# Optimization experiments

Measured on AMD Instinct MI355X. Metric: run time of the kernel, lower is better.

The kernel has to match this reference:

```python
import jax, jax.numpy as jnp
import numpy as np

N = 10000
E = 160000
UNITS = 64
NUM_RBF = 32
CUTOFF = 1.0


def _xavier(k, shape):
    fan_out, fan_in = shape
    lim = float(np.sqrt(6.0 / (fan_in + fan_out)))
    return jax.random.uniform(k, shape, minval=-lim, maxval=lim, dtype=jnp.float32)


def setup_inputs() -> dict:
    key = jax.random.key(0)
    ks = jax.random.split(key, 16)
    inp = {
        "edge_index": jax.random.randint(ks[0], (2, E), 0, N),
        "edge_weight": jax.random.uniform(ks[1], (E,), dtype=jnp.float32),
        "edge_attr": jax.random.normal(ks[2], (E, NUM_RBF), dtype=jnp.float32),
        "X": jax.random.normal(ks[3], (N, UNITS, 3, 3), dtype=jnp.float32),
        # scalar MLP: num_rbf -> units -> 2*units -> 3*units
        "Ws0": _xavier(ks[4], (UNITS, NUM_RBF)), "bs0": jnp.zeros((UNITS,), jnp.float32),
        "Ws1": _xavier(ks[5], (2 * UNITS, UNITS)), "bs1": jnp.zeros((2 * UNITS,), jnp.float32),
        "Ws2": _xavier(ks[6], (3 * UNITS, 2 * UNITS)), "bs2": jnp.zeros((3 * UNITS,), jnp.float32),
    }
    for i in range(6):
        inp[f"Wt{i}"] = _xavier(ks[7 + i], (UNITS, UNITS))
    return inp


def cosine_cutoff(r, cutoff):
    return jnp.where(r < cutoff, 0.5 * (jnp.cos(jnp.pi * r / cutoff) + 1.0), 0.0)


def tensor_norm(X):
    # X: [N, units, 3, 3] -> [N, units]
    return jnp.sum(X * X, axis=(-2, -1))


def decompose_tensor(X):
    eye = jnp.eye(3, dtype=X.dtype)
    trace = jnp.trace(X, axis1=-2, axis2=-1)  # [N, units]
    I = (trace / 3.0)[..., None, None] * eye
    A = 0.5 * (X - jnp.swapaxes(X, -2, -1))
    S = 0.5 * (X + jnp.swapaxes(X, -2, -1)) - I
    return I, A, S


def channel_linear(T, W):
    # linear over the channel dim: [N, c, 3, 3] x [d, c] -> [N, d, 3, 3]
    return jnp.einsum('ncij,dc->ndij', T, W)


def reference(edge_index, edge_weight, edge_attr, X,
              Ws0, bs0, Ws1, bs1, Ws2, bs2,
              Wt0, Wt1, Wt2, Wt3, Wt4, Wt5):
    act = jax.nn.silu
    C = cosine_cutoff(edge_weight, CUTOFF)  # [E]
    h = act(edge_attr @ Ws0.T + bs0)
    h = act(h @ Ws1.T + bs1)
    h = act(h @ Ws2.T + bs2)  # [E, 3*units]
    ea = (h * C[:, None]).reshape(h.shape[0], UNITS, 3)  # [E, units, 3]

    X = X / (tensor_norm(X) + 1.0)[..., None, None]
    I, A, S = decompose_tensor(X)
    I = channel_linear(I, Wt0)
    A = channel_linear(A, Wt1)
    S = channel_linear(S, Wt2)
    Y = I + A + S

    src, dst = edge_index[0], edge_index[1]
    n = X.shape[0]
    # message = per-edge radial scaling of gathered node tensors; aggregate at src
    Im = jax.ops.segment_sum(ea[..., 0, None, None] * I[dst], src, num_segments=n)
    Am = jax.ops.segment_sum(ea[..., 1, None, None] * A[dst], src, num_segments=n)
    Sm = jax.ops.segment_sum(ea[..., 2, None, None] * S[dst], src, num_segments=n)
    msg = Im + Am + Sm

    # O(3): symmetrized product of batched 3x3 matmuls
    AB = jnp.matmul(msg, Y) + jnp.matmul(Y, msg)
    I2, A2, S2 = decompose_tensor(AB)
    normp1 = (tensor_norm(I2 + A2 + S2) + 1.0)[..., None, None]
    I2 = channel_linear(I2 / normp1, Wt3)
    A2 = channel_linear(A2 / normp1, Wt4)
    S2 = channel_linear(S2 / normp1, Wt5)
    dX = I2 + A2 + S2
    return X + dX + jnp.matmul(dX, dX)
```

## Files before the change

### kernel.cpp

```cpp
#include <hip/hip_runtime.h>
#include <math.h>

#define NN 10000
#define EE 160000

#define OFF_WTT 0
#define OFF_PK  24576
#define OFF_B2P 41984
#define OFF_IASH 42176
#define OFF_EAH 3242176
#define OFF_ATTRP 18602176
#define OFF_CP  21162176
#define OFF_INT 21322176

typedef __attribute__((ext_vector_type(8))) _Float16 h16x8;
typedef __attribute__((ext_vector_type(2))) __fp16 fp16x2_raw;
typedef __attribute__((ext_vector_type(4))) float f32x4;

__device__ __forceinline__ float silu_f(float x) {
    return x * __builtin_amdgcn_rcpf(1.0f + __expf(-x));
}
__device__ __forceinline__ unsigned int pkh(float a, float b) {
    union { fp16x2_raw h; unsigned int u; } cv;
    cv.h = __builtin_amdgcn_cvt_pkrtz(a, b);
    return cv.u;
}
__device__ __forceinline__ unsigned short f2h(float f) {
    union { _Float16 h; unsigned short u; } cv; cv.h = (_Float16)f; return cv.u;
}
__device__ __forceinline__ float h2f(unsigned short s) {
    union { unsigned short u; _Float16 h; } cv; cv.u = s; return (float)cv.h;
}
__device__ __forceinline__ float h2f_lo(unsigned int u) { return h2f((unsigned short)(u & 0xffffu)); }
__device__ __forceinline__ float h2f_hi(unsigned int u) { return h2f((unsigned short)(u >> 16)); }
__device__ __forceinline__ unsigned int bperm(int addr, unsigned int v) {
    return (unsigned int)__builtin_amdgcn_ds_bpermute(addr, (int)v);
}

__global__ void k_prep(const float* __restrict__ Wt0, const float* __restrict__ Wt1,
                       const float* __restrict__ Wt2, const float* __restrict__ Wt3,
                       const float* __restrict__ Wt4, const float* __restrict__ Wt5,
                       const float* __restrict__ Ws0, const float* __restrict__ Ws1,
                       const float* __restrict__ Ws2, const float* __restrict__ bs2,
                       const int* __restrict__ ei,
                       float* __restrict__ WtT, unsigned short* __restrict__ PK,
                       float* __restrict__ bs2p, int* __restrict__ counts) {
    int idx = blockIdx.x * 256 + threadIdx.x;
    if (idx < 24576) {
        int k = idx >> 12, r = idx & 4095;
        int c = r >> 6, d = r & 63;
        const float* W = (k == 0) ? Wt0 : (k == 1) ? Wt1 : (k == 2) ? Wt2
                       : (k == 3) ? Wt3 : (k == 4) ? Wt4 : Wt5;
        WtT[idx] = W[d * 64 + c];
    } else if (idx < 26624) {
        int q = idx - 24576;
        int ot = q >> 9, r = q & 511, lane = r >> 3, j = r & 7;
        int k = ((lane >> 4) * 8) + j, o = ot * 16 + (lane & 15);
        PK[q] = f2h(Ws0[o * 32 + k]);
    } else if (idx < 34816) {
        int q = idx - 24576;
        int i = q - 2048, ch = i >> 9, r = i & 511, lane = r >> 3, j = r & 7;
        int ot = ch >> 1, ks = ch & 1;
        int k = ks * 32 + (lane >> 4) * 8 + j, o = ot * 16 + (lane & 15);
        PK[q] = f2h(Ws1[o * 64 + k]);
    } else if (idx < 59392) {
        int q = idx - 24576;
        int i = q - 10240, ch = i >> 9, r = i & 511, lane = r >> 3, j = r & 7;
        int ot = ch >> 2, ks = ch & 3;
        int k = ks * 32 + (lane >> 4) * 8 + j;
        int op = ot * 16 + (lane & 15);
        int o = (op & 63) * 3 + (op >> 6);
        PK[q] = f2h(Ws2[o * 128 + k]);
    } else if (idx < 59584) {
        int op = idx - 59392;
        bs2p[op] = bs2[(op & 63) * 3 + (op >> 6)];
    } else if (idx < 59584 + EE) {
        int e = idx - 59584;
        atomicAdd(&counts[ei[e]], 1);
    }
}

__global__ __launch_bounds__(256) void k_scan(const int* __restrict__ counts,
                                              int* __restrict__ offsets) {
    __shared__ int sums[256];
    int t = threadIdx.x;
    int base = t * 40;
    int s = 0;
    if (base < NN) {
        const int4* p = (const int4*)(counts + base);
#pragma unroll
        for (int q = 0; q < 10; ++q) { int4 a = p[q]; s += a.x + a.y + a.z + a.w; }
    }
    sums[t] = s;
    __syncthreads();
    for (int off = 1; off < 256; off <<= 1) {
        int tmp = (t >= off) ? sums[t - off] : 0;
        __syncthreads();
        sums[t] += tmp;
        __syncthreads();
    }
    int run = sums[t] - s;
    if (base < NN) {
        const int4* p = (const int4*)(counts + base);
#pragma unroll
        for (int q = 0; q < 10; ++q) {
            int4 a = p[q];
            offsets[base + 4 * q + 0] = run; run += a.x;
            offsets[base + 4 * q + 1] = run; run += a.y;
            offsets[base + 4 * q + 2] = run; run += a.z;
            offsets[base + 4 * q + 3] = run; run += a.w;
        }
    }
    if (t == 255) offsets[NN] = run;
}

__global__ void k_fill(const int* __restrict__ ei, const int* __restrict__ offsets,
                       const float* __restrict__ attr, const float* __restrict__ ew,
                       int* __restrict__ cursor, int* __restrict__ dstp,
                       unsigned short* __restrict__ attrP, float* __restrict__ Cp) {
    int e = blockIdx.x * 256 + threadIdx.x;
    if (e < EE) {
        int s = ei[e];
        int pos = offsets[s] + atomicAdd(&cursor[s], 1);
        dstp[pos] = ei[EE + e];
        const float4* ap = (const float4*)(attr + (size_t)e * 32);
        unsigned int pk[16];
#pragma unroll
        for (int q = 0; q < 8; ++q) {
            float4 v = ap[q];
            pk[2 * q]     = pkh(v.x, v.y);
            pk[2 * q + 1] = pkh(v.z, v.w);
        }
        uint4* dst = (uint4*)(attrP + (size_t)pos * 32);
#pragma unroll
        for (int q = 0; q < 4; ++q)
            dst[q] = make_uint4(pk[4 * q], pk[4 * q + 1], pk[4 * q + 2], pk[4 * q + 3]);
        float rw = ew[e];
        Cp[pos] = (rw < 1.0f) ? 0.5f * (cosf(3.14159265358979f * rw) + 1.0f) : 0.0f;
    }
}

__global__ __launch_bounds__(256) void k_nodeprep(const float* __restrict__ X,
                                                  const float* __restrict__ WtT,
                                                  unsigned int* __restrict__ IASu) {
    int t = threadIdx.x, w = t >> 6, c = t & 63;
    int n = blockIdx.x * 4 + w;
    __shared__ float XS[4][576];
    __shared__ float L[4][64][12];
    float* xs = XS[w];
#pragma unroll
    for (int i = 0; i < 9; i++) xs[c + 64 * i] = X[(size_t)n * 576 + c + 64 * i];
    __builtin_amdgcn_wave_barrier();
    float x[9];
#pragma unroll
    for (int j = 0; j < 9; j++) x[j] = xs[c * 9 + j];
    float nrm = 0.f;
#pragma unroll
    for (int j = 0; j < 9; j++) nrm += x[j] * x[j];
    float inv = __builtin_amdgcn_rcpf(nrm + 1.0f);
#pragma unroll
    for (int j = 0; j < 9; j++) x[j] *= inv;
    float tr3 = (x[0] + x[4] + x[8]) * (1.0f / 3.0f);
    L[w][c][0] = tr3;
    L[w][c][1] = 0.5f * (x[1] - x[3]);
    L[w][c][2] = 0.5f * (x[2] - x[6]);
    L[w][c][3] = 0.5f * (x[5] - x[7]);
    L[w][c][4] = x[0] - tr3;
    L[w][c][5] = x[4] - tr3;
    L[w][c][6] = 0.5f * (x[1] + x[3]);
    L[w][c][7] = 0.5f * (x[2] + x[6]);
    L[w][c][8] = 0.5f * (x[5] + x[7]);
    __builtin_amdgcn_wave_barrier();
    int d = c;
    const float* W0 = WtT;
    const float* W1 = WtT + 4096;
    const float* W2 = WtT + 8192;
    float aI = 0, aA0 = 0, aA1 = 0, aA2 = 0, aS0 = 0, aS1 = 0, aS2 = 0, aS3 = 0, aS4 = 0;
    for (int cc = 0; cc < 64; ++cc) {
        float w0 = W0[cc * 64 + d], w1 = W1[cc * 64 + d], w2 = W2[cc * 64 + d];
        float4 L0 = *(const float4*)&L[w][cc][0];
        float4 L1 = *(const float4*)&L[w][cc][4];
        float L8 = L[w][cc][8];
        aI  += w0 * L0.x;
        aA0 += w1 * L0.y; aA1 += w1 * L0.z; aA2 += w1 * L0.w;
        aS0 += w2 * L1.x; aS1 += w2 * L1.y; aS2 += w2 * L1.z;
        aS3 += w2 * L1.w; aS4 += w2 * L8;
    }
    unsigned int* op = IASu + (size_t)n * 320 + d;
    op[0]   = pkh(aI, aA0);
    op[64]  = pkh(aA1, aA2);
    op[128] = pkh(aS0, aS1);
    op[192] = pkh(aS2, aS3);
    op[256] = pkh(aS4, 0.0f);
}

__global__ __launch_bounds__(256) void k_mlp(const unsigned short* __restrict__ attrP,
                                             const float* __restrict__ Cp,
                                             const unsigned short* __restrict__ PK,
                                             const float* __restrict__ bs0,
                                             const float* __restrict__ bs1,
                                             const float* __restrict__ bs2p,
                                             unsigned short* __restrict__ eah) {
    int t = threadIdx.x, w = t >> 6, l = t & 63;
    int e = l & 15, lg = l >> 4;
    int pos = blockIdx.x * 64 + w * 16 + e;
    const h16x8* P1 = (const h16x8*)PK;
    const h16x8* P2 = (const h16x8*)(PK + 2048);
    const h16x8* P3 = (const h16x8*)(PK + 10240);
    union U8 { h16x8 h; unsigned int u[4]; uint4 v; };
    U8 B1;
    B1.v = *((const uint4*)(attrP + (size_t)pos * 32) + lg);
    float C = Cp[pos];
    int src0 = ((lg & 1) * 32 + e) * 4;
    int src1 = src0 + 64;
    bool hi = (lg >= 2);

    unsigned int h01[8], h23[8];
#pragma unroll
    for (int ot = 0; ot < 4; ++ot) {
        float4 bb = *(const float4*)&bs0[ot * 16 + lg * 4];
        f32x4 acc = {bb.x, bb.y, bb.z, bb.w};
        acc = __builtin_amdgcn_mfma_f32_16x16x32_f16(P1[ot * 64 + l], B1.h, acc, 0, 0, 0);
        h01[ot] = pkh(silu_f(acc[0]), silu_f(acc[1]));
        h23[ot] = pkh(silu_f(acc[2]), silu_f(acc[3]));
    }
    U8 B2a, B2b;
    {
        unsigned int a, b;
        a = bperm(src0, h01[0]); b = bperm(src0, h01[1]); B2a.u[0] = hi ? b : a;
        a = bperm(src0, h23[0]); b = bperm(src0, h23[1]); B2a.u[1] = hi ? b : a;
        a = bperm(src1, h01[0]); b = bperm(src1, h01[1]); B2a.u[2] = hi ? b : a;
        a = bperm(src1, h23[0]); b = bperm(src1, h23[1]); B2a.u[3] = hi ? b : a;
        a = bperm(src0, h01[2]); b = bperm(src0, h01[3]); B2b.u[0] = hi ? b : a;
        a = bperm(src0, h23[2]); b = bperm(src0, h23[3]); B2b.u[1] = hi ? b : a;
        a = bperm(src1, h01[2]); b = bperm(src1, h01[3]); B2b.u[2] = hi ? b : a;
        a = bperm(src1, h23[2]); b = bperm(src1, h23[3]); B2b.u[3] = hi ? b : a;
    }
#pragma unroll
    for (int ot = 0; ot < 8; ++ot) {
        float4 bb = *(const float4*)&bs1[ot * 16 + lg * 4];
        f32x4 acc = {bb.x, bb.y, bb.z, bb.w};
        acc = __builtin_amdgcn_mfma_f32_16x16x32_f16(P2[(ot * 2 + 0) * 64 + l], B2a.h, acc, 0, 0, 0);
        acc = __builtin_amdgcn_mfma_f32_16x16x32_f16(P2[(ot * 2 + 1) * 64 + l], B2b.h, acc, 0, 0, 0);
        h01[ot] = pkh(silu_f(acc[0]), silu_f(acc[1]));
        h23[ot] = pkh(silu_f(acc[2]), silu_f(acc[3]));
    }
    U8 B3[4];
#pragma unroll
    for (int ks = 0; ks < 4; ++ks) {
        unsigned int a, b;
        a = bperm(src0, h01[ks * 2]); b = bperm(src0, h01[ks * 2 + 1]); B3[ks].u[0] = hi ? b : a;
        a = bperm(src0, h23[ks * 2]); b = bperm(src0, h23[ks * 2 + 1]); B3[ks].u[1] = hi ? b : a;
        a = bperm(src1, h01[ks * 2]); b = bperm(src1, h01[ks * 2 + 1]); B3[ks].u[2] = hi ? b : a;
        a = bperm(src1, h23[ks * 2]); b = bperm(src1, h23[ks * 2 + 1]); B3[ks].u[3] = hi ? b : a;
    }
    size_t ebase = (size_t)pos * 192;
#pragma unroll
    for (int ot = 0; ot < 12; ++ot) {
        float4 bb = *(const float4*)&bs2p[ot * 16 + lg * 4];
        f32x4 acc = {bb.x, bb.y, bb.z, bb.w};
        acc = __builtin_amdgcn_mfma_f32_16x16x32_f16(P3[(ot * 4 + 0) * 64 + l], B3[0].h, acc, 0, 0, 0);
        acc = __builtin_amdgcn_mfma_f32_16x16x32_f16(P3[(ot * 4 + 1) * 64 + l], B3[1].h, acc, 0, 0, 0);
        acc = __builtin_amdgcn_mfma_f32_16x16x32_f16(P3[(ot * 4 + 2) * 64 + l], B3[2].h, acc, 0, 0, 0);
        acc = __builtin_amdgcn_mfma_f32_16x16x32_f16(P3[(ot * 4 + 3) * 64 + l], B3[3].h, acc, 0, 0, 0);
        unsigned int u01 = pkh(silu_f(acc[0]) * C, silu_f(acc[1]) * C);
        unsigned int u23 = pkh(silu_f(acc[2]) * C, silu_f(acc[3]) * C);
        *(uint2*)&eah[ebase + ot * 16 + lg * 4] = make_uint2(u01, u23);
    }
}

__global__ __launch_bounds__(256) void k_aggout(const int* __restrict__ offsets,
                                                const int* __restrict__ dstp,
                                                const unsigned short* __restrict__ eah,
                                                const unsigned int* __restrict__ IASu,
                                                const float* __restrict__ X,
                                                const float* __restrict__ WtT,
                                                float* __restrict__ out) {
    int t = threadIdx.x, w = t >> 6, c = t & 63;
    int n = blockIdx.x * 4 + w;
    __shared__ float XS[4][576];
    __shared__ float LO[4][768];
    float* xs = XS[w];
    float* lo = LO[w];
#pragma unroll
    for (int i = 0; i < 9; i++) xs[c + 64 * i] = X[(size_t)n * 576 + c + 64 * i];

    int beg = offsets[n], end = offsets[n + 1];
    float m0 = 0, m1 = 0, m2 = 0, m3 = 0, m4 = 0, m5 = 0, m6 = 0, m7 = 0, m8 = 0;
    int i = beg;
    for (; i + 4 <= end; i += 4) {
        float a[4][3];
        unsigned int u[4][5];
#pragma unroll
        for (int q = 0; q < 4; ++q) {
            const unsigned short* ep = eah + (size_t)(i + q) * 192;
            a[q][0] = h2f(ep[c]); a[q][1] = h2f(ep[64 + c]); a[q][2] = h2f(ep[128 + c]);
            const unsigned int* p = IASu + (size_t)dstp[i + q] * 320 + c;
            u[q][0] = p[0]; u[q][1] = p[64]; u[q][2] = p[128]; u[q][3] = p[192]; u[q][4] = p[256];
        }
#pragma unroll
        for (int q = 0; q < 4; ++q) {
            m0 += a[q][0] * h2f_lo(u[q][0]); m1 += a[q][1] * h2f_hi(u[q][0]);
            m2 += a[q][1] * h2f_lo(u[q][1]); m3 += a[q][1] * h2f_hi(u[q][1]);
            m4 += a[q][2] * h2f_lo(u[q][2]); m5 += a[q][2] * h2f_hi(u[q][2]);
            m6 += a[q][2] * h2f_lo(u[q][3]); m7 += a[q][2] * h2f_hi(u[q][3]);
            m8 += a[q][2] * h2f_lo(u[q][4]);
        }
    }
    for (; i < end; ++i) {
        const unsigned short* ep = eah + (size_t)i * 192;
        float a0 = h2f(ep[c]), a1 = h2f(ep[64 + c]), a2 = h2f(ep[128 + c]);
        const unsigned int* p = IASu + (size_t)dstp[i] * 320 + c;
        unsigned int u0 = p[0], u1 = p[64], u2 = p[128], u3 = p[192], u4 = p[256];
        m0 += a0 * h2f_lo(u0); m1 += a1 * h2f_hi(u0);
        m2 += a1 * h2f_lo(u1); m3 += a1 * h2f_hi(u1);
        m4 += a2 * h2f_lo(u2); m5 += a2 * h2f_hi(u2);
        m6 += a2 * h2f_lo(u3); m7 += a2 * h2f_hi(u3);
        m8 += a2 * h2f_lo(u4);
    }
    const unsigned int* yp = IASu + (size_t)n * 320 + c;
    unsigned int y0 = yp[0], y1 = yp[64], y2 = yp[128], y3 = yp[192], y4 = yp[256];
    float yI = h2f_lo(y0), yA0 = h2f_hi(y0), yA1 = h2f_lo(y1), yA2 = h2f_hi(y1);
    float yS0 = h2f_lo(y2), yS1 = h2f_hi(y2), yS2 = h2f_lo(y3), yS3 = h2f_hi(y3);
    float yS4 = h2f_lo(y4);

    float M[3][3] = {
        { m0 + m4,   m1 + m6,  m2 + m7 },
        { -m1 + m6,  m0 + m5,  m3 + m8 },
        { -m2 + m7, -m3 + m8,  m0 - m4 - m5 } };
    float Y[3][3] = {
        { yI + yS0,   yA0 + yS2,  yA1 + yS3 },
        { -yA0 + yS2, yI + yS1,   yA2 + yS4 },
        { -yA1 + yS3, -yA2 + yS4, yI - yS0 - yS1 } };
    float AB[3][3];
#pragma unroll
    for (int ii = 0; ii < 3; ii++)
#pragma unroll
        for (int j = 0; j < 3; j++) {
            float s = 0.f;
#pragma unroll
            for (int k = 0; k < 3; k++) s += M[ii][k] * Y[k][j] + Y[ii][k] * M[k][j];
            AB[ii][j] = s;
        }
    float tr3 = (AB[0][0] + AB[1][1] + AB[2][2]) * (1.0f / 3.0f);
    float fro = 0.f;
#pragma unroll
    for (int ii = 0; ii < 3; ii++)
#pragma unroll
        for (int j = 0; j < 3; j++) fro += AB[ii][j] * AB[ii][j];
    float inv = __builtin_amdgcn_rcpf(fro + 1.0f);
    float (*L12)[12] = (float (*)[12])lo;
    L12[c][0] = tr3 * inv;
    L12[c][1] = 0.5f * (AB[0][1] - AB[1][0]) * inv;
    L12[c][2] = 0.5f * (AB[0][2] - AB[2][0]) * inv;
    L12[c][3] = 0.5f * (AB[1][2] - AB[2][1]) * inv;
    L12[c][4] = (AB[0][0] - tr3) * inv;
    L12[c][5] = (AB[1][1] - tr3) * inv;
    L12[c][6] = 0.5f * (AB[0][1] + AB[1][0]) * inv;
    L12[c][7] = 0.5f * (AB[0][2] + AB[2][0]) * inv;
    L12[c][8] = 0.5f * (AB[1][2] + AB[2][1]) * inv;
    __builtin_amdgcn_wave_barrier();
    int d = c;
    const float* W3 = WtT + 3 * 4096;
    const float* W4 = WtT + 4 * 4096;
    const float* W5 = WtT + 5 * 4096;
    float aI = 0, aA0 = 0, aA1 = 0, aA2 = 0, aS0 = 0, aS1 = 0, aS2 = 0, aS3 = 0, aS4 = 0;
    for (int cc = 0; cc < 64; ++cc) {
        float w3 = W3[cc * 64 + d], w4 = W4[cc * 64 + d], w5 = W5[cc * 64 + d];
        float4 L0 = *(const float4*)&L12[cc][0];
        float4 L1 = *(const float4*)&L12[cc][4];
        float L8 = L12[cc][8];
        aI  += w3 * L0.x;
        aA0 += w4 * L0.y; aA1 += w4 * L0.z; aA2 += w4 * L0.w;
        aS0 += w5 * L1.x; aS1 += w5 * L1.y; aS2 += w5 * L1.z;
        aS3 += w5 * L1.w; aS4 += w5 * L8;
    }
    float dX[3][3] = {
        { aI + aS0,   aA0 + aS2,  aA1 + aS3 },
        { -aA0 + aS2, aI + aS1,   aA2 + aS4 },
        { -aA1 + aS3, -aA2 + aS4, aI - aS0 - aS1 } };
    float D2[3][3];
#pragma unroll
    for (int ii = 0; ii < 3; ii++)
#pragma unroll
        for (int j = 0; j < 3; j++) {
            float s = 0.f;
#pragma unroll
            for (int k = 0; k < 3; k++) s += dX[ii][k] * dX[k][j];
            D2[ii][j] = s;
        }
    float x[9];
    __builtin_amdgcn_wave_barrier();
#pragma unroll
    for (int j = 0; j < 9; j++) x[j] = xs[d * 9 + j];
    float nrm = 0.f;
#pragma unroll
    for (int j = 0; j < 9; j++) nrm += x[j] * x[j];
    float xinv = __builtin_amdgcn_rcpf(nrm + 1.0f);
    __builtin_amdgcn_wave_barrier();
#pragma unroll
    for (int ii = 0; ii < 3; ii++)
#pragma unroll
        for (int j = 0; j < 3; j++)
            lo[d * 9 + ii * 3 + j] = x[ii * 3 + j] * xinv + dX[ii][j] + D2[ii][j];
    __builtin_amdgcn_wave_barrier();
#pragma unroll
    for (int ii = 0; ii < 9; ii++) out[(size_t)n * 576 + c + 64 * ii] = lo[c + 64 * ii];
}

extern "C" void kernel_launch(void* const* d_in, const int* in_sizes, int n_in,
                              void* d_out, int out_size, void* d_ws, size_t ws_size,
                              hipStream_t stream) {
    (void)in_sizes; (void)n_in; (void)out_size; (void)ws_size;
    const int* ei = (const int*)d_in[0];
    const float* ew = (const float*)d_in[1];
    const float* attr = (const float*)d_in[2];
    const float* X = (const float*)d_in[3];
    const float* Ws0 = (const float*)d_in[4];
    const float* bs0 = (const float*)d_in[5];
    const float* Ws1 = (const float*)d_in[6];
    const float* bs1 = (const float*)d_in[7];
    const float* Ws2 = (const float*)d_in[8];
    const float* bs2 = (const float*)d_in[9];
    const float* Wt0 = (const float*)d_in[10];
    const float* Wt1 = (const float*)d_in[11];
    const float* Wt2 = (const float*)d_in[12];
    const float* Wt3 = (const float*)d_in[13];
    const float* Wt4 = (const float*)d_in[14];
    const float* Wt5 = (const float*)d_in[15];
    float* ws = (float*)d_ws;
    int* ibase = (int*)(ws + OFF_INT);
    int* counts = ibase;
    int* cursor = ibase + NN;
    int* offsets = ibase + 2 * NN;
    int* dstp = ibase + 3 * NN + 1;
    unsigned short* PK = (unsigned short*)(ws + OFF_PK);
    unsigned int* IASu = (unsigned int*)(ws + OFF_IASH);
    unsigned short* eah = (unsigned short*)(ws + OFF_EAH);
    unsigned short* attrP = (unsigned short*)(ws + OFF_ATTRP);
    float* Cp = ws + OFF_CP;

    (void)hipMemsetAsync(counts, 0, 2 * NN * sizeof(int), stream);
    k_prep<<<(59584 + EE + 255) / 256, 256, 0, stream>>>(
        Wt0, Wt1, Wt2, Wt3, Wt4, Wt5, Ws0, Ws1, Ws2, bs2, ei,
        ws, PK, ws + OFF_B2P, counts);
    k_scan<<<1, 256, 0, stream>>>(counts, offsets);
    k_fill<<<(EE + 255) / 256, 256, 0, stream>>>(ei, offsets, attr, ew, cursor, dstp, attrP, Cp);
    k_nodeprep<<<NN / 4, 256, 0, stream>>>(X, ws, IASu);
    k_mlp<<<EE / 64, 256, 0, stream>>>(attrP, Cp, PK, bs0, bs1, ws + OFF_B2P, eah);
    k_aggout<<<NN / 4, 256, 0, stream>>>(offsets, dstp, eah, IASu, X, ws, (float*)d_out);
}
```

Measured before the change: 160.0 us.

## Run edge MLP in original edge order and gather via bucket index in aggregation

The fill kernel no longer permutes and converts edge attributes and cutoff values into sorted order. It only records the original edge id per sorted slot. The MLP now reads fp32 attributes and edge weights directly in original order, converting to fp16 and computing the cosine cutoff itself. The aggregation kernel gathers per-edge MLP outputs through the bucket indirection instead of reading them contiguously, and gains an 8-way unrolled loop for more loads in flight. This removes a scatter and an intermediate buffer but makes the eah reads in aggregation random.

```diff
diff --git a/kernel.cpp b/kernel.cpp
--- a/kernel.cpp
+++ b/kernel.cpp
@@ -9,9 +9,7 @@
 #define OFF_B2P 41984
 #define OFF_IASH 42176
 #define OFF_EAH 3242176
-#define OFF_ATTRP 18602176
-#define OFF_CP  21162176
-#define OFF_INT 21322176
+#define OFF_INT 18602176
 
 typedef __attribute__((ext_vector_type(8))) _Float16 h16x8;
 typedef __attribute__((ext_vector_type(2))) __fp16 fp16x2_raw;
@@ -115,28 +113,14 @@
 }
 
 __global__ void k_fill(const int* __restrict__ ei, const int* __restrict__ offsets,
-                       const float* __restrict__ attr, const float* __restrict__ ew,
-                       int* __restrict__ cursor, int* __restrict__ dstp,
-                       unsigned short* __restrict__ attrP, float* __restrict__ Cp) {
+                       int* __restrict__ cursor, int* __restrict__ bucket,
+                       int* __restrict__ dstp) {
     int e = blockIdx.x * 256 + threadIdx.x;
     if (e < EE) {
         int s = ei[e];
         int pos = offsets[s] + atomicAdd(&cursor[s], 1);
+        bucket[pos] = e;
         dstp[pos] = ei[EE + e];
-        const float4* ap = (const float4*)(attr + (size_t)e * 32);
-        unsigned int pk[16];
-#pragma unroll
-        for (int q = 0; q < 8; ++q) {
-            float4 v = ap[q];
-            pk[2 * q]     = pkh(v.x, v.y);
-            pk[2 * q + 1] = pkh(v.z, v.w);
-        }
-        uint4* dst = (uint4*)(attrP + (size_t)pos * 32);
-#pragma unroll
-        for (int q = 0; q < 4; ++q)
-            dst[q] = make_uint4(pk[4 * q], pk[4 * q + 1], pk[4 * q + 2], pk[4 * q + 3]);
-        float rw = ew[e];
-        Cp[pos] = (rw < 1.0f) ? 0.5f * (cosf(3.14159265358979f * rw) + 1.0f) : 0.0f;
     }
 }
 
@@ -194,8 +178,8 @@
     op[256] = pkh(aS4, 0.0f);
 }
 
-__global__ __launch_bounds__(256) void k_mlp(const unsigned short* __restrict__ attrP,
-                                             const float* __restrict__ Cp,
+__global__ __launch_bounds__(256) void k_mlp(const float* __restrict__ attr,
+                                             const float* __restrict__ ew,
                                              const unsigned short* __restrict__ PK,
                                              const float* __restrict__ bs0,
                                              const float* __restrict__ bs1,
@@ -209,8 +193,15 @@
     const h16x8* P3 = (const h16x8*)(PK + 10240);
     union U8 { h16x8 h; unsigned int u[4]; uint4 v; };
     U8 B1;
-    B1.v = *((const uint4*)(attrP + (size_t)pos * 32) + lg);
-    float C = Cp[pos];
+    {
+        const float* ap = attr + (size_t)pos * 32 + lg * 8;
+        float4 a0 = *(const float4*)ap;
+        float4 a1 = *(const float4*)(ap + 4);
+        B1.u[0] = pkh(a0.x, a0.y); B1.u[1] = pkh(a0.z, a0.w);
+        B1.u[2] = pkh(a1.x, a1.y); B1.u[3] = pkh(a1.z, a1.w);
+    }
+    float rw = ew[pos];
+    float C = (rw < 1.0f) ? 0.5f * (cosf(3.14159265358979f * rw) + 1.0f) : 0.0f;
     int src0 = ((lg & 1) * 32 + e) * 4;
     int src1 = src0 + 64;
     bool hi = (lg >= 2);
@@ -270,6 +261,7 @@
 }
 
 __global__ __launch_bounds__(256) void k_aggout(const int* __restrict__ offsets,
+                                                const int* __restrict__ bucket,
                                                 const int* __restrict__ dstp,
                                                 const unsigned short* __restrict__ eah,
                                                 const unsigned int* __restrict__ IASu,
@@ -288,12 +280,31 @@
     int beg = offsets[n], end = offsets[n + 1];
     float m0 = 0, m1 = 0, m2 = 0, m3 = 0, m4 = 0, m5 = 0, m6 = 0, m7 = 0, m8 = 0;
     int i = beg;
+    for (; i + 8 <= end; i += 8) {
+        float a[8][3];
+        unsigned int u[8][5];
+#pragma unroll
+        for (int q = 0; q < 8; ++q) {
+            const unsigned short* ep = eah + (size_t)bucket[i + q] * 192;
+            a[q][0] = h2f(ep[c]); a[q][1] = h2f(ep[64 + c]); a[q][2] = h2f(ep[128 + c]);
+            const unsigned int* p = IASu + (size_t)dstp[i + q] * 320 + c;
+            u[q][0] = p[0]; u[q][1] = p[64]; u[q][2] = p[128]; u[q][3] = p[192]; u[q][4] = p[256];
+        }
+#pragma unroll
+        for (int q = 0; q < 8; ++q) {
+            m0 += a[q][0] * h2f_lo(u[q][0]); m1 += a[q][1] * h2f_hi(u[q][0]);
+            m2 += a[q][1] * h2f_lo(u[q][1]); m3 += a[q][1] * h2f_hi(u[q][1]);
+            m4 += a[q][2] * h2f_lo(u[q][2]); m5 += a[q][2] * h2f_hi(u[q][2]);
+            m6 += a[q][2] * h2f_lo(u[q][3]); m7 += a[q][2] * h2f_hi(u[q][3]);
+            m8 += a[q][2] * h2f_lo(u[q][4]);
+        }
+    }
     for (; i + 4 <= end; i += 4) {
         float a[4][3];
         unsigned int u[4][5];
 #pragma unroll
         for (int q = 0; q < 4; ++q) {
-            const unsigned short* ep = eah + (size_t)(i + q) * 192;
+            const unsigned short* ep = eah + (size_t)bucket[i + q] * 192;
             a[q][0] = h2f(ep[c]); a[q][1] = h2f(ep[64 + c]); a[q][2] = h2f(ep[128 + c]);
             const unsigned int* p = IASu + (size_t)dstp[i + q] * 320 + c;
             u[q][0] = p[0]; u[q][1] = p[64]; u[q][2] = p[128]; u[q][3] = p[192]; u[q][4] = p[256];
@@ -308,7 +319,7 @@
         }
     }
     for (; i < end; ++i) {
-        const unsigned short* ep = eah + (size_t)i * 192;
+        const unsigned short* ep = eah + (size_t)bucket[i] * 192;
         float a0 = h2f(ep[c]), a1 = h2f(ep[64 + c]), a2 = h2f(ep[128 + c]);
         const unsigned int* p = IASu + (size_t)dstp[i] * 320 + c;
         unsigned int u0 = p[0], u1 = p[64], u2 = p[128], u3 = p[192], u4 = p[256];
@@ -433,20 +444,19 @@
     int* counts = ibase;
     int* cursor = ibase + NN;
     int* offsets = ibase + 2 * NN;
-    int* dstp = ibase + 3 * NN + 1;
+    int* bucket = ibase + 3 * NN + 1;
+    int* dstp = bucket + EE;
     unsigned short* PK = (unsigned short*)(ws + OFF_PK);
     unsigned int* IASu = (unsigned int*)(ws + OFF_IASH);
     unsigned short* eah = (unsigned short*)(ws + OFF_EAH);
-    unsigned short* attrP = (unsigned short*)(ws + OFF_ATTRP);
-    float* Cp = ws + OFF_CP;
 
     (void)hipMemsetAsync(counts, 0, 2 * NN * sizeof(int), stream);
     k_prep<<<(59584 + EE + 255) / 256, 256, 0, stream>>>(
         Wt0, Wt1, Wt2, Wt3, Wt4, Wt5, Ws0, Ws1, Ws2, bs2, ei,
         ws, PK, ws + OFF_B2P, counts);
     k_scan<<<1, 256, 0, stream>>>(counts, offsets);
-    k_fill<<<(EE + 255) / 256, 256, 0, stream>>>(ei, offsets, attr, ew, cursor, dstp, attrP, Cp);
+    k_fill<<<(EE + 255) / 256, 256, 0, stream>>>(ei, offsets, cursor, bucket, dstp);
     k_nodeprep<<<NN / 4, 256, 0, stream>>>(X, ws, IASu);
-    k_mlp<<<EE / 64, 256, 0, stream>>>(attrP, Cp, PK, bs0, bs1, ws + OFF_B2P, eah);
-    k_aggout<<<NN / 4, 256, 0, stream>>>(offsets, dstp, eah, IASu, X, ws, (float*)d_out);
-}
+    k_mlp<<<EE / 64, 256, 0, stream>>>(attr, ew, PK, bs0, bs1, ws + OFF_B2P, eah);
+    k_aggout<<<NN / 4, 256, 0, stream>>>(offsets, bucket, dstp, eah, IASu, X, ws, (float*)d_out);
+}
```

Result: no change. 161.9 us (+1.2%).

## Merge node-prep and edge MLP into one launch; shuffle-broadcast dst indices

Applied to the files above, without the earlier changes.

Folds the node-preparation kernel and the edge MLP kernel into a single launch whose block index picks which job each block does, so one launch and its tail disappear and the two independent workloads can overlap on the GPU. In the aggregation kernel each wave now loads up to 64 destination indices at once and broadcasts them with shuffles, replacing repeated scalar-dependent global loads inside the gather loop. The fused kernel reserves the larger node-prep shared memory for every block, which may reduce occupancy for the MLP blocks.

```diff
diff --git a/kernel.cpp b/kernel.cpp
--- a/kernel.cpp
+++ b/kernel.cpp
@@ -140,132 +140,133 @@
     }
 }
 
-__global__ __launch_bounds__(256) void k_nodeprep(const float* __restrict__ X,
-                                                  const float* __restrict__ WtT,
-                                                  unsigned int* __restrict__ IASu) {
-    int t = threadIdx.x, w = t >> 6, c = t & 63;
-    int n = blockIdx.x * 4 + w;
-    __shared__ float XS[4][576];
-    __shared__ float L[4][64][12];
-    float* xs = XS[w];
-#pragma unroll
-    for (int i = 0; i < 9; i++) xs[c + 64 * i] = X[(size_t)n * 576 + c + 64 * i];
-    __builtin_amdgcn_wave_barrier();
-    float x[9];
-#pragma unroll
-    for (int j = 0; j < 9; j++) x[j] = xs[c * 9 + j];
-    float nrm = 0.f;
-#pragma unroll
-    for (int j = 0; j < 9; j++) nrm += x[j] * x[j];
-    float inv = __builtin_amdgcn_rcpf(nrm + 1.0f);
-#pragma unroll
-    for (int j = 0; j < 9; j++) x[j] *= inv;
-    float tr3 = (x[0] + x[4] + x[8]) * (1.0f / 3.0f);
-    L[w][c][0] = tr3;
-    L[w][c][1] = 0.5f * (x[1] - x[3]);
-    L[w][c][2] = 0.5f * (x[2] - x[6]);
-    L[w][c][3] = 0.5f * (x[5] - x[7]);
-    L[w][c][4] = x[0] - tr3;
-    L[w][c][5] = x[4] - tr3;
-    L[w][c][6] = 0.5f * (x[1] + x[3]);
-    L[w][c][7] = 0.5f * (x[2] + x[6]);
-    L[w][c][8] = 0.5f * (x[5] + x[7]);
-    __builtin_amdgcn_wave_barrier();
-    int d = c;
-    const float* W0 = WtT;
-    const float* W1 = WtT + 4096;
-    const float* W2 = WtT + 8192;
-    float aI = 0, aA0 = 0, aA1 = 0, aA2 = 0, aS0 = 0, aS1 = 0, aS2 = 0, aS3 = 0, aS4 = 0;
-    for (int cc = 0; cc < 64; ++cc) {
-        float w0 = W0[cc * 64 + d], w1 = W1[cc * 64 + d], w2 = W2[cc * 64 + d];
-        float4 L0 = *(const float4*)&L[w][cc][0];
-        float4 L1 = *(const float4*)&L[w][cc][4];
-        float L8 = L[w][cc][8];
-        aI  += w0 * L0.x;
-        aA0 += w1 * L0.y; aA1 += w1 * L0.z; aA2 += w1 * L0.w;
-        aS0 += w2 * L1.x; aS1 += w2 * L1.y; aS2 += w2 * L1.z;
-        aS3 += w2 * L1.w; aS4 += w2 * L8;
-    }
-    unsigned int* op = IASu + (size_t)n * 320 + d;
-    op[0]   = pkh(aI, aA0);
-    op[64]  = pkh(aA1, aA2);
-    op[128] = pkh(aS0, aS1);
-    op[192] = pkh(aS2, aS3);
-    op[256] = pkh(aS4, 0.0f);
-}
-
-__global__ __launch_bounds__(256) void k_mlp(const unsigned short* __restrict__ attrP,
-                                             const float* __restrict__ Cp,
-                                             const unsigned short* __restrict__ PK,
-                                             const float* __restrict__ bs0,
-                                             const float* __restrict__ bs1,
-                                             const float* __restrict__ bs2p,
-                                             unsigned short* __restrict__ eah) {
+__global__ __launch_bounds__(256) void k_mlpnp(const unsigned short* __restrict__ attrP,
+                                               const float* __restrict__ Cp,
+                                               const unsigned short* __restrict__ PK,
+                                               const float* __restrict__ bs0,
+                                               const float* __restrict__ bs1,
+                                               const float* __restrict__ bs2p,
+                                               const float* __restrict__ X,
+                                               const float* __restrict__ WtT,
+                                               unsigned short* __restrict__ eah,
+                                               unsigned int* __restrict__ IASu) {
+    __shared__ float SH[4][1344];
     int t = threadIdx.x, w = t >> 6, l = t & 63;
-    int e = l & 15, lg = l >> 4;
-    int pos = blockIdx.x * 64 + w * 16 + e;
-    const h16x8* P1 = (const h16x8*)PK;
-    const h16x8* P2 = (const h16x8*)(PK + 2048);
-    const h16x8* P3 = (const h16x8*)(PK + 10240);
-    union U8 { h16x8 h; unsigned int u[4]; uint4 v; };
-    U8 B1;
-    B1.v = *((const uint4*)(attrP + (size_t)pos * 32) + lg);
-    float C = Cp[pos];
-    int src0 = ((lg & 1) * 32 + e) * 4;
-    int src1 = src0 + 64;
-    bool hi = (lg >= 2);
-
-    unsigned int h01[8], h23[8];
-#pragma unroll
-    for (int ot = 0; ot < 4; ++ot) {
-        float4 bb = *(const float4*)&bs0[ot * 16 + lg * 4];
-        f32x4 acc = {bb.x, bb.y, bb.z, bb.w};
-        acc = __builtin_amdgcn_mfma_f32_16x16x32_f16(P1[ot * 64 + l], B1.h, acc, 0, 0, 0);
-        h01[ot] = pkh(silu_f(acc[0]), silu_f(acc[1]));
-        h23[ot] = pkh(silu_f(acc[2]), silu_f(acc[3]));
-    }
-    U8 B2a, B2b;
-    {
-        unsigned int a, b;
-        a = bperm(src0, h01[0]); b = bperm(src0, h01[1]); B2a.u[0] = hi ? b : a;
-        a = bperm(src0, h23[0]); b = bperm(src0, h23[1]); B2a.u[1] = hi ? b : a;
-        a = bperm(src1, h01[0]); b = bperm(src1, h01[1]); B2a.u[2] = hi ? b : a;
-        a = bperm(src1, h23[0]); b = bperm(src1, h23[1]); B2a.u[3] = hi ? b : a;
-        a = bperm(src0, h01[2]); b = bperm(src0, h01[3]); B2b.u[0] = hi ? b : a;
-        a = bperm(src0, h23[2]); b = bperm(src0, h23[3]); B2b.u[1] = hi ? b : a;
-        a = bperm(src1, h01[2]); b = bperm(src1, h01[3]); B2b.u[2] = hi ? b : a;
-        a = bperm(src1, h23[2]); b = bperm(src1, h23[3]); B2b.u[3] = hi ? b : a;
-    }
-#pragma unroll
-    for (int ot = 0; ot < 8; ++ot) {
-        float4 bb = *(const float4*)&bs1[ot * 16 + lg * 4];
-        f32x4 acc = {bb.x, bb.y, bb.z, bb.w};
-        acc = __builtin_amdgcn_mfma_f32_16x16x32_f16(P2[(ot * 2 + 0) * 64 + l], B2a.h, acc, 0, 0, 0);
-        acc = __builtin_amdgcn_mfma_f32_16x16x32_f16(P2[(ot * 2 + 1) * 64 + l], B2b.h, acc, 0, 0, 0);
-        h01[ot] = pkh(silu_f(acc[0]), silu_f(acc[1]));
-        h23[ot] = pkh(silu_f(acc[2]), silu_f(acc[3]));
-    }
-    U8 B3[4];
-#pragma unroll
-    for (int ks = 0; ks < 4; ++ks) {
-        unsigned int a, b;
-        a = bperm(src0, h01[ks * 2]); b = bperm(src0, h01[ks * 2 + 1]); B3[ks].u[0] = hi ? b : a;
-        a = bperm(src0, h23[ks * 2]); b = bperm(src0, h23[ks * 2 + 1]); B3[ks].u[1] = hi ? b : a;
-        a = bperm(src1, h01[ks * 2]); b = bperm(src1, h01[ks * 2 + 1]); B3[ks].u[2] = hi ? b : a;
-        a = bperm(src1, h23[ks * 2]); b = bperm(src1, h23[ks * 2 + 1]); B3[ks].u[3] = hi ? b : a;
-    }
-    size_t ebase = (size_t)pos * 192;
-#pragma unroll
-    for (int ot = 0; ot < 12; ++ot) {
-        float4 bb = *(const float4*)&bs2p[ot * 16 + lg * 4];
-        f32x4 acc = {bb.x, bb.y, bb.z, bb.w};
-        acc = __builtin_amdgcn_mfma_f32_16x16x32_f16(P3[(ot * 4 + 0) * 64 + l], B3[0].h, acc, 0, 0, 0);
-        acc = __builtin_amdgcn_mfma_f32_16x16x32_f16(P3[(ot * 4 + 1) * 64 + l], B3[1].h, acc, 0, 0, 0);
-        acc = __builtin_amdgcn_mfma_f32_16x16x32_f16(P3[(ot * 4 + 2) * 64 + l], B3[2].h, acc, 0, 0, 0);
-        acc = __builtin_amdgcn_mfma_f32_16x16x32_f16(P3[(ot * 4 + 3) * 64 + l], B3[3].h, acc, 0, 0, 0);
-        unsigned int u01 = pkh(silu_f(acc[0]) * C, silu_f(acc[1]) * C);
-        unsigned int u23 = pkh(silu_f(acc[2]) * C, silu_f(acc[3]) * C);
-        *(uint2*)&eah[ebase + ot * 16 + lg * 4] = make_uint2(u01, u23);
+    if (blockIdx.x < EE / 64) {
+        int e = l & 15, lg = l >> 4;
+        int pos = blockIdx.x * 64 + w * 16 + e;
+        const h16x8* P1 = (const h16x8*)PK;
+        const h16x8* P2 = (const h16x8*)(PK + 2048);
+        const h16x8* P3 = (const h16x8*)(PK + 10240);
+        union U8 { h16x8 h; unsigned int u[4]; uint4 v; };
+        U8 B1;
+        B1.v = *((const uint4*)(attrP + (size_t)pos * 32) + lg);
+        float C = Cp[pos];
+        int src0 = ((lg & 1) * 32 + e) * 4;
+        int src1 = src0 + 64;
+        bool hi = (lg >= 2);
+
+        unsigned int h01[8], h23[8];
+#pragma unroll
+        for (int ot = 0; ot < 4; ++ot) {
+            float4 bb = *(const float4*)&bs0[ot * 16 + lg * 4];
+            f32x4 acc = {bb.x, bb.y, bb.z, bb.w};
+            acc = __builtin_amdgcn_mfma_f32_16x16x32_f16(P1[ot * 64 + l], B1.h, acc, 0, 0, 0);
+            h01[ot] = pkh(silu_f(acc[0]), silu_f(acc[1]));
+            h23[ot] = pkh(silu_f(acc[2]), silu_f(acc[3]));
+        }
+        U8 B2a, B2b;
+        {
+            unsigned int a, b;
+            a = bperm(src0, h01[0]); b = bperm(src0, h01[1]); B2a.u[0] = hi ? b : a;
+            a = bperm(src0, h23[0]); b = bperm(src0, h23[1]); B2a.u[1] = hi ? b : a;
+            a = bperm(src1, h01[0]); b = bperm(src1, h01[1]); B2a.u[2] = hi ? b : a;
+            a = bperm(src1, h23[0]); b = bperm(src1, h23[1]); B2a.u[3] = hi ? b : a;
+            a = bperm(src0, h01[2]); b = bperm(src0, h01[3]); B2b.u[0] = hi ? b : a;
+            a = bperm(src0, h23[2]); b = bperm(src0, h23[3]); B2b.u[1] = hi ? b : a;
+            a = bperm(src1, h01[2]); b = bperm(src1, h01[3]); B2b.u[2] = hi ? b : a;
+            a = bperm(src1, h23[2]); b = bperm(src1, h23[3]); B2b.u[3] = hi ? b : a;
+        }
+#pragma unroll
+        for (int ot = 0; ot < 8; ++ot) {
+            float4 bb = *(const float4*)&bs1[ot * 16 + lg * 4];
+            f32x4 acc = {bb.x, bb.y, bb.z, bb.w};
+            acc = __builtin_amdgcn_mfma_f32_16x16x32_f16(P2[(ot * 2 + 0) * 64 + l], B2a.h, acc, 0, 0, 0);
+            acc = __builtin_amdgcn_mfma_f32_16x16x32_f16(P2[(ot * 2 + 1) * 64 + l], B2b.h, acc, 0, 0, 0);
+            h01[ot] = pkh(silu_f(acc[0]), silu_f(acc[1]));
+            h23[ot] = pkh(silu_f(acc[2]), silu_f(acc[3]));
+        }
+        U8 B3[4];
+#pragma unroll
+        for (int ks = 0; ks < 4; ++ks) {
+            unsigned int a, b;
+            a = bperm(src0, h01[ks * 2]); b = bperm(src0, h01[ks * 2 + 1]); B3[ks].u[0] = hi ? b : a;
+            a = bperm(src0, h23[ks * 2]); b = bperm(src0, h23[ks * 2 + 1]); B3[ks].u[1] = hi ? b : a;
+            a = bperm(src1, h01[ks * 2]); b = bperm(src1, h01[ks * 2 + 1]); B3[ks].u[2] = hi ? b : a;
+            a = bperm(src1, h23[ks * 2]); b = bperm(src1, h23[ks * 2 + 1]); B3[ks].u[3] = hi ? b : a;
+        }
+        size_t ebase = (size_t)pos * 192;
+#pragma unroll
+        for (int ot = 0; ot < 12; ++ot) {
+            float4 bb = *(const float4*)&bs2p[ot * 16 + lg * 4];
+            f32x4 acc = {bb.x, bb.y, bb.z, bb.w};
+            acc = __builtin_amdgcn_mfma_f32_16x16x32_f16(P3[(ot * 4 + 0) * 64 + l], B3[0].h, acc, 0, 0, 0);
+            acc = __builtin_amdgcn_mfma_f32_16x16x32_f16(P3[(ot * 4 + 1) * 64 + l], B3[1].h, acc, 0, 0, 0);
+            acc = __builtin_amdgcn_mfma_f32_16x16x32_f16(P3[(ot * 4 + 2) * 64 + l], B3[2].h, acc, 0, 0, 0);
+            acc = __builtin_amdgcn_mfma_f32_16x16x32_f16(P3[(ot * 4 + 3) * 64 + l], B3[3].h, acc, 0, 0, 0);
+            unsigned int u01 = pkh(silu_f(acc[0]) * C, silu_f(acc[1]) * C);
+            unsigned int u23 = pkh(silu_f(acc[2]) * C, silu_f(acc[3]) * C);
+            *(uint2*)&eah[ebase + ot * 16 + lg * 4] = make_uint2(u01, u23);
+        }
+    } else {
+        int c = l;
+        int n = (blockIdx.x - EE / 64) * 4 + w;
+        float* xs = SH[w];
+        float (*L12)[12] = (float (*)[12])(xs + 576);
+#pragma unroll
+        for (int i = 0; i < 9; i++) xs[c + 64 * i] = X[(size_t)n * 576 + c + 64 * i];
+        __builtin_amdgcn_wave_barrier();
+        float x[9];
+#pragma unroll
+        for (int j = 0; j < 9; j++) x[j] = xs[c * 9 + j];
+        float nrm = 0.f;
+#pragma unroll
+        for (int j = 0; j < 9; j++) nrm += x[j] * x[j];
+        float inv = __builtin_amdgcn_rcpf(nrm + 1.0f);
+#pragma unroll
+        for (int j = 0; j < 9; j++) x[j] *= inv;
+        float tr3 = (x[0] + x[4] + x[8]) * (1.0f / 3.0f);
+        L12[c][0] = tr3;
+        L12[c][1] = 0.5f * (x[1] - x[3]);
+        L12[c][2] = 0.5f * (x[2] - x[6]);
+        L12[c][3] = 0.5f * (x[5] - x[7]);
+        L12[c][4] = x[0] - tr3;
+        L12[c][5] = x[4] - tr3;
+        L12[c][6] = 0.5f * (x[1] + x[3]);
+        L12[c][7] = 0.5f * (x[2] + x[6]);
+        L12[c][8] = 0.5f * (x[5] + x[7]);
+        __builtin_amdgcn_wave_barrier();
+        int d = c;
+        const float* W0 = WtT;
+        const float* W1 = WtT + 4096;
+        const float* W2 = WtT + 8192;
+        float aI = 0, aA0 = 0, aA1 = 0, aA2 = 0, aS0 = 0, aS1 = 0, aS2 = 0, aS3 = 0, aS4 = 0;
+        for (int cc = 0; cc < 64; ++cc) {
+            float w0 = W0[cc * 64 + d], w1 = W1[cc * 64 + d], w2 = W2[cc * 64 + d];
+            float4 L0 = *(const float4*)&L12[cc][0];
+            float4 L1 = *(const float4*)&L12[cc][4];
+            float L8 = L12[cc][8];
+            aI  += w0 * L0.x;
+            aA0 += w1 * L0.y; aA1 += w1 * L0.z; aA2 += w1 * L0.w;
+            aS0 += w2 * L1.x; aS1 += w2 * L1.y; aS2 += w2 * L1.z;
+            aS3 += w2 * L1.w; aS4 += w2 * L8;
+        }
+        unsigned int* op = IASu + (size_t)n * 320 + d;
+        op[0]   = pkh(aI, aA0);
+        op[64]  = pkh(aA1, aA2);
+        op[128] = pkh(aS0, aS1);
+        op[192] = pkh(aS2, aS3);
+        op[256] = pkh(aS4, 0.0f);
     }
 }
 
@@ -286,16 +287,24 @@
     for (int i = 0; i < 9; i++) xs[c + 64 * i] = X[(size_t)n * 576 + c + 64 * i];
 
     int beg = offsets[n], end = offsets[n + 1];
+    int dv = 0;
+    { int idx = beg + c; if (idx < end) dv = dstp[idx]; }
     float m0 = 0, m1 = 0, m2 = 0, m3 = 0, m4 = 0, m5 = 0, m6 = 0, m7 = 0, m8 = 0;
     int i = beg;
     for (; i + 4 <= end; i += 4) {
+        int q0 = i - beg;
+        int d0 = (q0 < 64)     ? __shfl(dv, q0)     : dstp[i];
+        int d1 = (q0 + 1 < 64) ? __shfl(dv, q0 + 1) : dstp[i + 1];
+        int d2 = (q0 + 2 < 64) ? __shfl(dv, q0 + 2) : dstp[i + 2];
+        int d3 = (q0 + 3 < 64) ? __shfl(dv, q0 + 3) : dstp[i + 3];
+        int dd[4] = {d0, d1, d2, d3};
         float a[4][3];
         unsigned int u[4][5];
 #pragma unroll
         for (int q = 0; q < 4; ++q) {
             const unsigned short* ep = eah + (size_t)(i + q) * 192;
             a[q][0] = h2f(ep[c]); a[q][1] = h2f(ep[64 + c]); a[q][2] = h2f(ep[128 + c]);
-            const unsigned int* p = IASu + (size_t)dstp[i + q] * 320 + c;
+            const unsigned int* p = IASu + (size_t)dd[q] * 320 + c;
             u[q][0] = p[0]; u[q][1] = p[64]; u[q][2] = p[128]; u[q][3] = p[192]; u[q][4] = p[256];
         }
 #pragma unroll
@@ -308,9 +317,11 @@
         }
     }
     for (; i < end; ++i) {
+        int q0 = i - beg;
+        int dst = (q0 < 64) ? __shfl(dv, q0) : dstp[i];
         const unsigned short* ep = eah + (size_t)i * 192;
         float a0 = h2f(ep[c]), a1 = h2f(ep[64 + c]), a2 = h2f(ep[128 + c]);
-        const unsigned int* p = IASu + (size_t)dstp[i] * 320 + c;
+        const unsigned int* p = IASu + (size_t)dst * 320 + c;
         unsigned int u0 = p[0], u1 = p[64], u2 = p[128], u3 = p[192], u4 = p[256];
         m0 += a0 * h2f_lo(u0); m1 += a1 * h2f_hi(u0);
         m2 += a1 * h2f_lo(u1); m3 += a1 * h2f_hi(u1);
@@ -446,7 +457,7 @@
         ws, PK, ws + OFF_B2P, counts);
     k_scan<<<1, 256, 0, stream>>>(counts, offsets);
     k_fill<<<(EE + 255) / 256, 256, 0, stream>>>(ei, offsets, attr, ew, cursor, dstp, attrP, Cp);
-    k_nodeprep<<<NN / 4, 256, 0, stream>>>(X, ws, IASu);
-    k_mlp<<<EE / 64, 256, 0, stream>>>(attrP, Cp, PK, bs0, bs1, ws + OFF_B2P, eah);
+    k_mlpnp<<<EE / 64 + NN / 4, 256, 0, stream>>>(attrP, Cp, PK, bs0, bs1, ws + OFF_B2P,
+                                                  X, ws, eah, IASu);
     k_aggout<<<NN / 4, 256, 0, stream>>>(offsets, dstp, eah, IASu, X, ws, (float*)d_out);
 }
```

New measurement: 160.9 us. Within noise of the previous version (+0.6%).
